# Optimization experiments

Measured on AMD Instinct MI355X. Metric: run time of the kernel, lower is better.

Reference implementation:

```python
import jax, jax.numpy as jnp
import numpy as np

N = 20000
E = 320000
NEG_SLOPE = 0.2
LN_EPS = 1e-5


def gat_conv(x, W, a_src, a_dst, b, src, dst, heads, ch, concat):
    # x: [N, F_in]; W: [F_in, H*C]; a_src/a_dst: [H, C]; b: [H*C] or [C]
    xl = (x @ W).reshape(N, heads, ch)                      # [N,H,C]
    alpha_src = jnp.sum(xl * a_src, axis=-1)                # [N,H]
    alpha_dst = jnp.sum(xl * a_dst, axis=-1)                # [N,H]
    e = alpha_src[src] + alpha_dst[dst]                     # [E',H]
    e = jax.nn.leaky_relu(e, NEG_SLOPE)
    # segment softmax over incoming edges of each dst node
    m = jax.ops.segment_max(e, dst, num_segments=N)         # [N,H]
    m = jnp.where(jnp.isfinite(m), m, 0.0)
    ex = jnp.exp(e - m[dst])
    denom = jax.ops.segment_sum(ex, dst, num_segments=N)    # [N,H]
    alpha = ex / (denom[dst] + 1e-16)                       # [E',H]
    msg = alpha[:, :, None] * xl[src]                       # [E',H,C]
    out = jax.ops.segment_sum(msg, dst, num_segments=N)     # [N,H,C]
    if concat:
        return out.reshape(N, heads * ch) + b
    return out.mean(axis=1) + b


def layer_norm(x, g, b):
    mu = jnp.mean(x, axis=-1, keepdims=True)
    var = jnp.mean(jnp.square(x - mu), axis=-1, keepdims=True)
    return (x - mu) * jax.lax.rsqrt(var + LN_EPS) * g + b


def setup_inputs() -> dict:
    key = jax.random.key(0)
    ks = jax.random.split(key, 24)
    d = {}
    d["x"] = jax.random.normal(ks[0], (N, 50), dtype=jnp.float32)
    d["edge_index"] = jax.random.randint(ks[1], (2, E), 0, N, dtype=jnp.int64)

    def glorot(k, shape):
        fan = shape[0] + shape[-1]
        return jax.random.normal(k, shape, dtype=jnp.float32) * np.sqrt(2.0 / fan)

    # conv1: 50 -> 256, heads=4, concat
    d["W1"] = glorot(ks[2], (50, 4 * 256))
    d["a_src1"] = glorot(ks[3], (4, 256))
    d["a_dst1"] = glorot(ks[4], (4, 256))
    d["b1"] = jnp.zeros((4 * 256,), jnp.float32)
    # conv2: 1024 -> 256, heads=4, concat
    d["W2"] = glorot(ks[5], (1024, 4 * 256))
    d["a_src2"] = glorot(ks[6], (4, 256))
    d["a_dst2"] = glorot(ks[7], (4, 256))
    d["b2"] = jnp.zeros((4 * 256,), jnp.float32)
    # conv3: 1024 -> 121, heads=6, concat=False
    d["W3"] = glorot(ks[8], (1024, 6 * 121))
    d["a_src3"] = glorot(ks[9], (6, 121))
    d["a_dst3"] = glorot(ks[10], (6, 121))
    d["b3"] = jnp.zeros((121,), jnp.float32)
    # skips
    d["skipW1"] = glorot(ks[11], (50, 1024))
    d["skipb1"] = jnp.zeros((1024,), jnp.float32)
    d["skipW2"] = glorot(ks[12], (1024, 1024))
    d["skipb2"] = jnp.zeros((1024,), jnp.float32)
    # layer norms
    d["g1"] = jnp.ones((1024,), jnp.float32)
    d["beta1"] = jnp.zeros((1024,), jnp.float32)
    d["g2"] = jnp.ones((1024,), jnp.float32)
    d["beta2"] = jnp.zeros((1024,), jnp.float32)
    return d


def reference(x, edge_index, W1, a_src1, a_dst1, b1, W2, a_src2, a_dst2, b2,
              W3, a_src3, a_dst3, b3, skipW1, skipb1, skipW2, skipb2,
              g1, beta1, g2, beta2):
    # add self loops (PyG GATConv default)
    loop = jnp.arange(N, dtype=edge_index.dtype)
    src = jnp.concatenate([edge_index[0], loop])
    dst = jnp.concatenate([edge_index[1], loop])

    h = gat_conv(x, W1, a_src1, a_dst1, b1, src, dst, 4, 256, True)
    h = jax.nn.elu(layer_norm(h + (x @ skipW1 + skipb1), g1, beta1))
    h2 = gat_conv(h, W2, a_src2, a_dst2, b2, src, dst, 4, 256, True)
    h2 = jax.nn.elu(layer_norm(h2 + (h @ skipW2 + skipb2), g2, beta2))
    out = gat_conv(h2, W3, a_src3, a_dst3, b3, src, dst, 6, 121, False)
    return out
```

## Files before the change

### kernel.cpp

```cpp
#include <hip/hip_runtime.h>
#include <hip/hip_bf16.h>
#include <math.h>

typedef __attribute__((ext_vector_type(8))) __bf16 bf16x8;
typedef __attribute__((ext_vector_type(2))) __bf16 bf16x2;
typedef __attribute__((ext_vector_type(4))) float f32x4;

#define LSTR 40

__global__ __launch_bounds__(256) void gemm_bt(const __bf16* __restrict__ A,
                                               const __bf16* __restrict__ Bt,
                                               __bf16* __restrict__ C,
                                               int M, int N, int K) {
    __shared__ __bf16 As[128 * LSTR];
    __shared__ __bf16 Bs[128 * LSTR];
    const int t = threadIdx.x;
    const int lane = t & 63;
    const int wid = t >> 6;
    const int wm = (wid >> 1) << 6;
    const int wn = (wid & 1) << 6;
    const int bm = blockIdx.x * 128;
    const int bn = blockIdx.y * 128;

    const int lr = t >> 2;
    const int lc = (t & 3) << 3;

    f32x4 acc[4][4];
#pragma unroll
    for (int i = 0; i < 4; i++)
#pragma unroll
        for (int j = 0; j < 4; j++) acc[i][j] = (f32x4){0.f, 0.f, 0.f, 0.f};

    const int m16 = lane & 15;
    const int k8 = (lane >> 4) << 3;

    for (int k0 = 0; k0 < K; k0 += 32) {
        bf16x8 a0 = *(const bf16x8*)(A + (size_t)(bm + lr) * K + k0 + lc);
        bf16x8 a1 = *(const bf16x8*)(A + (size_t)(bm + lr + 64) * K + k0 + lc);
        bf16x8 b0 = *(const bf16x8*)(Bt + (size_t)(bn + lr) * K + k0 + lc);
        bf16x8 b1 = *(const bf16x8*)(Bt + (size_t)(bn + lr + 64) * K + k0 + lc);
        __syncthreads();
        *(bf16x8*)(As + lr * LSTR + lc) = a0;
        *(bf16x8*)(As + (lr + 64) * LSTR + lc) = a1;
        *(bf16x8*)(Bs + lr * LSTR + lc) = b0;
        *(bf16x8*)(Bs + (lr + 64) * LSTR + lc) = b1;
        __syncthreads();
        bf16x8 af[4], bfr[4];
#pragma unroll
        for (int i = 0; i < 4; i++) {
            af[i] = *(const bf16x8*)(As + (wm + 16 * i + m16) * LSTR + k8);
            bfr[i] = *(const bf16x8*)(Bs + (wn + 16 * i + m16) * LSTR + k8);
        }
#pragma unroll
        for (int i = 0; i < 4; i++)
#pragma unroll
            for (int j = 0; j < 4; j++)
                acc[i][j] = __builtin_amdgcn_mfma_f32_16x16x32_bf16(af[i], bfr[j], acc[i][j], 0, 0, 0);
    }
    const int r4 = (lane >> 4) << 2;
#pragma unroll
    for (int i = 0; i < 4; i++) {
#pragma unroll
        for (int j = 0; j < 4; j++) {
            int col = bn + wn + 16 * j + m16;
#pragma unroll
            for (int r = 0; r < 4; r++) {
                int row = bm + wm + 16 * i + r4 + r;
                C[(size_t)row * N + col] = (__bf16)acc[i][j][r];
            }
        }
    }
}

__global__ void pack_x_k(const float* __restrict__ x, __bf16* __restrict__ xp, int rows_real) {
    int i = blockIdx.x * 256 + threadIdx.x;
    int n = i >> 6, c = i & 63;
    float v = 0.f;
    if (n < rows_real && c < 50) v = x[n * 50 + c];
    xp[(size_t)n * 64 + c] = (__bf16)v;
}

__global__ void transpose_pad_k(const float* __restrict__ W, __bf16* __restrict__ WT,
                                int K, int N, int Kp, int Np) {
    __shared__ float tile[32][33];
    int bx = blockIdx.x, by = blockIdx.y;
    int tx = threadIdx.x & 31, ty = threadIdx.x >> 5;
#pragma unroll
    for (int r = ty; r < 32; r += 8) {
        int k = by * 32 + r, n = bx * 32 + tx;
        float v = 0.f;
        if (k < K && n < N) v = W[(size_t)k * N + n];
        tile[r][tx] = v;
    }
    __syncthreads();
#pragma unroll
    for (int r = ty; r < 32; r += 8) {
        int n = bx * 32 + r, k = by * 32 + tx;
        if (n < Np && k < Kp) WT[(size_t)n * Kp + k] = (__bf16)tile[tx][r];
    }
}

__global__ void probe_ei_k(const int* __restrict__ ei, int* __restrict__ flag) {
    if (blockIdx.x == 0 && threadIdx.x == 0) {
        int all0 = 1;
        for (int i = 0; i < 64; i++)
            if (ei[2 * i + 1] != 0) { all0 = 0; break; }
        *flag = all0;
    }
}

__device__ __forceinline__ int load_ei(const int* ei, int idx, int is64) {
    return is64 ? ei[2 * idx] : ei[idx];
}

__global__ void hist_k(const int* __restrict__ ei, const int* __restrict__ flag,
                       int* __restrict__ cnt, int E, int Nn) {
    int e = blockIdx.x * 256 + threadIdx.x;
    if (e >= E + Nn) return;
    int is64 = *flag;
    int d = (e < E) ? load_ei(ei, E + e, is64) : (e - E);
    d = min(max(d, 0), Nn - 1);
    atomicAdd(&cnt[d], 1);
}

__global__ __launch_bounds__(1024) void scan_k(const int* __restrict__ cnt, int* __restrict__ row_ptr,
                                               int Nn, int total) {
    __shared__ int part[1024];
    int t = threadIdx.x;
    int chunk = (Nn + 1023) >> 10;
    int lo = t * chunk;
    int hi = lo + chunk; if (hi > Nn) hi = Nn; if (lo > Nn) lo = Nn;
    int s = 0;
    for (int i = lo; i < hi; i++) s += cnt[i];
    part[t] = s;
    __syncthreads();
    for (int off = 1; off < 1024; off <<= 1) {
        int v = (t >= off) ? part[t - off] : 0;
        __syncthreads();
        part[t] += v;
        __syncthreads();
    }
    int run = part[t] - s;
    for (int i = lo; i < hi; i++) { row_ptr[i] = run; run += cnt[i]; }
    if (t == 0) row_ptr[Nn] = total;
}

__global__ void fill_csr_k(const int* __restrict__ ei, const int* __restrict__ flag,
                           const int* __restrict__ row_ptr, int* __restrict__ cursor,
                           int* __restrict__ src_csr, int E, int Nn) {
    int e = blockIdx.x * 256 + threadIdx.x;
    if (e >= E + Nn) return;
    int is64 = *flag;
    int d = (e < E) ? load_ei(ei, E + e, is64) : (e - E);
    int s = (e < E) ? load_ei(ei, e, is64) : (e - E);
    d = min(max(d, 0), Nn - 1);
    s = min(max(s, 0), Nn - 1);
    int slot = row_ptr[d] + atomicAdd(&cursor[d], 1);
    src_csr[slot] = s;
}

__global__ void alpha_k(const __bf16* __restrict__ XL, int ld, const float* __restrict__ a_src,
                        const float* __restrict__ a_dst, float* __restrict__ asrc,
                        float* __restrict__ adst, int Nn, int H, int C, int Cpad) {
    int gw = (blockIdx.x * 256 + threadIdx.x) >> 6;
    int lane = threadIdx.x & 63;
    if (gw >= Nn * H) return;
    int n = gw / H, h = gw - n * H;
    const __bf16* row = XL + (size_t)n * ld + h * Cpad;
    const float* as = a_src + h * C;
    const float* ad = a_dst + h * C;
    float s = 0.f, d = 0.f;
    for (int c = lane; c < C; c += 64) {
        float v = (float)row[c];
        s += v * as[c];
        d += v * ad[c];
    }
#pragma unroll
    for (int off = 32; off; off >>= 1) {
        s += __shfl_down(s, off);
        d += __shfl_down(d, off);
    }
    if (lane == 0) { asrc[n * H + h] = s; adst[n * H + h] = d; }
}

__global__ void attn_k(const int* __restrict__ row_ptr, const int* __restrict__ src_csr,
                       const float* __restrict__ asrc, const float* __restrict__ adst,
                       float* __restrict__ w, int Nn, int H) {
    int gw = (blockIdx.x * 256 + threadIdx.x) >> 6;
    int lane = threadIdx.x & 63;
    if (gw >= Nn) return;
    int n = gw;
    int base = row_ptr[n], deg = row_ptr[n + 1] - base;
    for (int h = 0; h < H; h++) {
        float ad = adst[n * H + h];
        float m = -1e30f;
        for (int s = lane; s < deg; s += 64) {
            float e = asrc[src_csr[base + s] * H + h] + ad;
            e = e > 0.f ? e : 0.2f * e;
            m = fmaxf(m, e);
        }
#pragma unroll
        for (int off = 1; off < 64; off <<= 1) m = fmaxf(m, __shfl_xor(m, off));
        float sum = 0.f;
        for (int s = lane; s < deg; s += 64) {
            float e = asrc[src_csr[base + s] * H + h] + ad;
            e = e > 0.f ? e : 0.2f * e;
            sum += __expf(e - m);
        }
#pragma unroll
        for (int off = 1; off < 64; off <<= 1) sum += __shfl_xor(sum, off);
        float inv = 1.f / (sum + 1e-16f);
        for (int s = lane; s < deg; s += 64) {
            float e = asrc[src_csr[base + s] * H + h] + ad;
            e = e > 0.f ? e : 0.2f * e;
            w[(size_t)(base + s) * H + h] = __expf(e - m) * inv;
        }
    }
}

__global__ __launch_bounds__(256) void agg_skip4(const __bf16* __restrict__ XL,
                                                 const float* __restrict__ w,
                                                 const int* __restrict__ row_ptr,
                                                 const int* __restrict__ src_csr,
                                                 const float* __restrict__ bias,
                                                 const float* __restrict__ sb,
                                                 __bf16* __restrict__ SK, int Nn) {
    const int cc = blockIdx.x;
    const int n = blockIdx.y * 4 + (threadIdx.x >> 6);
    const int lane = threadIdx.x & 63;
    if (n >= Nn) return;
    const int g = lane >> 4;
    const int p = lane & 15;
    const int col = cc * 128 + p * 8;
    const int head = cc >> 1;
    const int base = row_ptr[n], end = row_ptr[n + 1];

    float acc[8];
#pragma unroll
    for (int j = 0; j < 8; j++) acc[j] = 0.f;

    for (int e = base; e < end; e += 8) {
        int ea = e + g, eb = e + g + 4;
        bool va = ea < end, vb = eb < end;
        int sa = va ? src_csr[ea] : src_csr[base];
        int sb2 = vb ? src_csr[eb] : src_csr[base];
        float wa = va ? w[(size_t)ea * 4 + head] : 0.f;
        float wb = vb ? w[(size_t)eb * 4 + head] : 0.f;
        bf16x8 xa = *(const bf16x8*)(XL + (size_t)sa * 1024 + col);
        bf16x8 xb = *(const bf16x8*)(XL + (size_t)sb2 * 1024 + col);
#pragma unroll
        for (int j = 0; j < 8; j++) acc[j] += wa * (float)xa[j] + wb * (float)xb[j];
    }
#pragma unroll
    for (int j = 0; j < 8; j++) {
        acc[j] += __shfl_xor(acc[j], 16);
        acc[j] += __shfl_xor(acc[j], 32);
    }
    if (lane < 16) {
        size_t o = (size_t)n * 1024 + col;
        bf16x8 sk = *(const bf16x8*)(SK + o);
        bf16x8 res;
#pragma unroll
        for (int j = 0; j < 8; j++)
            res[j] = (__bf16)(acc[j] + bias[col + j] + sb[col + j] + (float)sk[j]);
        *(bf16x8*)(SK + o) = res;
    }
}

__global__ __launch_bounds__(256) void agg_mean4(const __bf16* __restrict__ XL,
                                                 const float* __restrict__ w,
                                                 const int* __restrict__ row_ptr,
                                                 const int* __restrict__ src_csr,
                                                 __bf16* __restrict__ part, int Nn) {
    const int cc = blockIdx.x;
    const int n = blockIdx.y * 4 + (threadIdx.x >> 6);
    const int lane = threadIdx.x & 63;
    if (n >= Nn) return;
    const int g = lane >> 4;
    const int p = lane & 15;
    int col = cc * 96 + p * 8;
    if (col > 760) col = 760;
    const int h0 = col / 121;
    int h1 = (col + 7) / 121;
    if (h1 > 5) h1 = 5;
    bool hi[8];
#pragma unroll
    for (int j = 0; j < 8; j++) hi[j] = ((col + j) / 121) > h0;
    const int base = row_ptr[n], end = row_ptr[n + 1];

    float acc[8];
#pragma unroll
    for (int j = 0; j < 8; j++) acc[j] = 0.f;

    for (int e = base; e < end; e += 8) {
        int ea = e + g, eb = e + g + 4;
        bool va = ea < end, vb = eb < end;
        int sa = va ? src_csr[ea] : src_csr[base];
        int sb2 = vb ? src_csr[eb] : src_csr[base];
        const float* wpa = w + (size_t)ea * 6;
        const float* wpb = w + (size_t)eb * 6;
        float wa0 = va ? wpa[h0] : 0.f, wa1 = va ? wpa[h1] : 0.f;
        float wb0 = vb ? wpb[h0] : 0.f, wb1 = vb ? wpb[h1] : 0.f;
        bf16x8 xa = *(const bf16x8*)(XL + (size_t)sa * 768 + col);
        bf16x8 xb = *(const bf16x8*)(XL + (size_t)sb2 * 768 + col);
#pragma unroll
        for (int j = 0; j < 8; j++) {
            float wja = hi[j] ? wa1 : wa0;
            float wjb = hi[j] ? wb1 : wb0;
            acc[j] += wja * (float)xa[j] + wjb * (float)xb[j];
        }
    }
#pragma unroll
    for (int j = 0; j < 8; j++) {
        acc[j] += __shfl_xor(acc[j], 16);
        acc[j] += __shfl_xor(acc[j], 32);
    }
    if (lane < 12) {
        size_t o = (size_t)n * 768 + cc * 96 + lane * 8;
        bf16x8 res;
#pragma unroll
        for (int j = 0; j < 8; j++) res[j] = (__bf16)acc[j];
        *(bf16x8*)(part + o) = res;
    }
}

__global__ __launch_bounds__(128) void reduce_mean_k(const __bf16* __restrict__ part,
                                                     const float* __restrict__ b3,
                                                     float* __restrict__ out, int Nn) {
    int n = blockIdx.x;
    int t = threadIdx.x;
    if (t >= 121) return;
    const __bf16* row = part + (size_t)n * 768;
    float s = 0.f;
#pragma unroll
    for (int h = 0; h < 6; h++) s += (float)row[h * 121 + t];
    out[(size_t)n * 121 + t] = s * (1.f / 6.f) + b3[t];
}

__global__ __launch_bounds__(256) void ln_elu_k(const __bf16* __restrict__ in,
                                                const float* __restrict__ g,
                                                const float* __restrict__ be,
                                                __bf16* __restrict__ out, int rows_real) {
    const int D = 1024;
    int n = blockIdx.x;
    int t = threadIdx.x;
    size_t ro = (size_t)n * D;
    if (n >= rows_real) {
#pragma unroll
        for (int j = 0; j < 4; j++) out[ro + t + 256 * j] = (__bf16)0.f;
        return;
    }
    float v[4];
    float s = 0.f, q = 0.f;
#pragma unroll
    for (int j = 0; j < 4; j++) {
        int c = t + 256 * j;
        float a = (float)in[ro + c];
        v[j] = a;
        s += a;
        q += a * a;
    }
#pragma unroll
    for (int off = 32; off; off >>= 1) {
        s += __shfl_down(s, off);
        q += __shfl_down(q, off);
    }
    __shared__ float rs[8];
    int wid = t >> 6;
    if ((t & 63) == 0) { rs[wid] = s; rs[wid + 4] = q; }
    __syncthreads();
    s = rs[0] + rs[1] + rs[2] + rs[3];
    q = rs[4] + rs[5] + rs[6] + rs[7];
    float mu = s * (1.f / 1024.f);
    float var = q * (1.f / 1024.f) - mu * mu;
    float inv = rsqrtf(fmaxf(var, 0.f) + 1e-5f);
#pragma unroll
    for (int j = 0; j < 4; j++) {
        int c = t + 256 * j;
        float y = (v[j] - mu) * inv * g[c] + be[c];
        y = y > 0.f ? y : expm1f(y);
        out[ro + c] = (__bf16)y;
    }
}

extern "C" void kernel_launch(void* const* d_in, const int* in_sizes, int n_in,
                              void* d_out, int out_size, void* d_ws, size_t ws_size,
                              hipStream_t stream) {
    const float* x   = (const float*)d_in[0];
    const int*   ei  = (const int*)d_in[1];
    const float* W1  = (const float*)d_in[2];
    const float* as1 = (const float*)d_in[3];
    const float* ad1 = (const float*)d_in[4];
    const float* b1  = (const float*)d_in[5];
    const float* W2  = (const float*)d_in[6];
    const float* as2 = (const float*)d_in[7];
    const float* ad2 = (const float*)d_in[8];
    const float* b2  = (const float*)d_in[9];
    const float* W3  = (const float*)d_in[10];
    const float* as3 = (const float*)d_in[11];
    const float* ad3 = (const float*)d_in[12];
    const float* b3  = (const float*)d_in[13];
    const float* sW1 = (const float*)d_in[14];
    const float* sb1 = (const float*)d_in[15];
    const float* sW2 = (const float*)d_in[16];
    const float* sb2 = (const float*)d_in[17];
    const float* g1  = (const float*)d_in[18];
    const float* be1 = (const float*)d_in[19];
    const float* g2  = (const float*)d_in[20];
    const float* be2 = (const float*)d_in[21];
    float* out = (float*)d_out;

    const int Nn = 20000;
    const int E = in_sizes[1] / 2;
    const int E2 = E + Nn;
    const int Mpad = 20096;

    char* p = (char*)d_ws;
    auto alloc = [&](size_t bytes) {
        char* r = p;
        p += (bytes + 255) & ~(size_t)255;
        return r;
    };
    __bf16* W1pT  = (__bf16*)alloc((size_t)1024 * 64 * 2);
    __bf16* sW1T  = (__bf16*)alloc((size_t)1024 * 64 * 2);
    __bf16* W2T   = (__bf16*)alloc((size_t)1024 * 1024 * 2);
    __bf16* sW2T  = (__bf16*)alloc((size_t)1024 * 1024 * 2);
    __bf16* W3pT  = (__bf16*)alloc((size_t)768 * 1024 * 2);
    __bf16* xp    = (__bf16*)alloc((size_t)Mpad * 64 * 2);
    __bf16* XL    = (__bf16*)alloc((size_t)Mpad * 1024 * 2);
    __bf16* SK    = (__bf16*)alloc((size_t)Mpad * 1024 * 2);
    __bf16* H1    = (__bf16*)alloc((size_t)Mpad * 1024 * 2);
    float*  asrcb = (float*)alloc((size_t)Nn * 6 * 4);
    float*  adstb = (float*)alloc((size_t)Nn * 6 * 4);
    float*  wbuf  = (float*)alloc((size_t)E2 * 6 * 4);
    int*    rowp  = (int*)alloc((size_t)(Nn + 1) * 4);
    int*    cnt   = (int*)alloc((size_t)Nn * 4);
    int*    scsr  = (int*)alloc((size_t)E2 * 4);
    int*    eiflag= (int*)alloc(256);
    __bf16* part  = SK;
    (void)ws_size; (void)n_in; (void)out_size;

    pack_x_k<<<(Mpad * 64) / 256, 256, 0, stream>>>(x, xp, Nn);
    transpose_pad_k<<<dim3(32, 2), 256, 0, stream>>>(W1, W1pT, 50, 1024, 64, 1024);
    transpose_pad_k<<<dim3(32, 2), 256, 0, stream>>>(sW1, sW1T, 50, 1024, 64, 1024);
    transpose_pad_k<<<dim3(32, 32), 256, 0, stream>>>(W2, W2T, 1024, 1024, 1024, 1024);
    transpose_pad_k<<<dim3(32, 32), 256, 0, stream>>>(sW2, sW2T, 1024, 1024, 1024, 1024);
    transpose_pad_k<<<dim3(24, 32), 256, 0, stream>>>(W3, W3pT, 1024, 726, 1024, 768);

    probe_ei_k<<<1, 64, 0, stream>>>(ei, eiflag);
    hipMemsetAsync(cnt, 0, (size_t)Nn * 4, stream);
    hist_k<<<(E2 + 255) / 256, 256, 0, stream>>>(ei, eiflag, cnt, E, Nn);
    scan_k<<<1, 1024, 0, stream>>>(cnt, rowp, Nn, E2);
    hipMemsetAsync(cnt, 0, (size_t)Nn * 4, stream);
    fill_csr_k<<<(E2 + 255) / 256, 256, 0, stream>>>(ei, eiflag, rowp, cnt, scsr, E, Nn);

    gemm_bt<<<dim3(Mpad / 128, 8), 256, 0, stream>>>(xp, W1pT, XL, Mpad, 1024, 64);
    gemm_bt<<<dim3(Mpad / 128, 8), 256, 0, stream>>>(xp, sW1T, SK, Mpad, 1024, 64);
    alpha_k<<<(Nn * 4 * 64) / 256, 256, 0, stream>>>(XL, 1024, as1, ad1, asrcb, adstb, Nn, 4, 256, 256);
    attn_k<<<(Nn + 3) / 4, 256, 0, stream>>>(rowp, scsr, asrcb, adstb, wbuf, Nn, 4);
    agg_skip4<<<dim3(8, (Nn + 3) / 4), 256, 0, stream>>>(XL, wbuf, rowp, scsr, b1, sb1, SK, Nn);
    ln_elu_k<<<Mpad, 256, 0, stream>>>(SK, g1, be1, H1, Nn);

    gemm_bt<<<dim3(Mpad / 128, 8), 256, 0, stream>>>(H1, W2T, XL, Mpad, 1024, 1024);
    gemm_bt<<<dim3(Mpad / 128, 8), 256, 0, stream>>>(H1, sW2T, SK, Mpad, 1024, 1024);
    alpha_k<<<(Nn * 4 * 64) / 256, 256, 0, stream>>>(XL, 1024, as2, ad2, asrcb, adstb, Nn, 4, 256, 256);
    attn_k<<<(Nn + 3) / 4, 256, 0, stream>>>(rowp, scsr, asrcb, adstb, wbuf, Nn, 4);
    agg_skip4<<<dim3(8, (Nn + 3) / 4), 256, 0, stream>>>(XL, wbuf, rowp, scsr, b2, sb2, SK, Nn);
    ln_elu_k<<<Mpad, 256, 0, stream>>>(SK, g2, be2, H1, Nn);

    gemm_bt<<<dim3(Mpad / 128, 6), 256, 0, stream>>>(H1, W3pT, XL, Mpad, 768, 1024);
    alpha_k<<<(Nn * 6 * 64) / 256, 256, 0, stream>>>(XL, 768, as3, ad3, asrcb, adstb, Nn, 6, 121, 121);
    attn_k<<<(Nn + 3) / 4, 256, 0, stream>>>(rowp, scsr, asrcb, adstb, wbuf, Nn, 6);
    agg_mean4<<<dim3(8, (Nn + 3) / 4), 256, 0, stream>>>(XL, wbuf, rowp, scsr, part, Nn);
    reduce_mean_k<<<Nn, 128, 0, stream>>>(part, b3, out, Nn);
}
```

Baseline: 869.6 us.

## Use direct global-to-LDS loads in GEMM, pad layer-3 heads, widen aggregation

```diff
diff --git a/kernel.cpp b/kernel.cpp
--- a/kernel.cpp
+++ b/kernel.cpp
@@ -3,17 +3,24 @@
 #include <math.h>
 
 typedef __attribute__((ext_vector_type(8))) __bf16 bf16x8;
-typedef __attribute__((ext_vector_type(2))) __bf16 bf16x2;
 typedef __attribute__((ext_vector_type(4))) float f32x4;
 
-#define LSTR 40
+#if __has_builtin(__builtin_amdgcn_global_load_lds)
+#define HAVE_GLD 1
+#define GLD16(g, l)                                                                      \
+    __builtin_amdgcn_global_load_lds(                                                    \
+        (const __attribute__((address_space(1))) unsigned int*)(g),                      \
+        (__attribute__((address_space(3))) unsigned int*)(l), 16, 0, 0)
+#else
+#define HAVE_GLD 0
+#endif
 
 __global__ __launch_bounds__(256) void gemm_bt(const __bf16* __restrict__ A,
                                                const __bf16* __restrict__ Bt,
                                                __bf16* __restrict__ C,
                                                int M, int N, int K) {
-    __shared__ __bf16 As[128 * LSTR];
-    __shared__ __bf16 Bs[128 * LSTR];
+    __shared__ __bf16 As[128 * 32];
+    __shared__ __bf16 Bs[128 * 32];
     const int t = threadIdx.x;
     const int lane = t & 63;
     const int wid = t >> 6;
@@ -22,8 +29,8 @@
     const int bm = blockIdx.x * 128;
     const int bn = blockIdx.y * 128;
 
-    const int lr = t >> 2;
-    const int lc = (t & 3) << 3;
+    const int srow = (wid << 4) + (lane >> 2);
+    const int scol = (lane & 3) << 3;
 
     f32x4 acc[4][4];
 #pragma unroll
@@ -35,21 +42,30 @@
     const int k8 = (lane >> 4) << 3;
 
     for (int k0 = 0; k0 < K; k0 += 32) {
-        bf16x8 a0 = *(const bf16x8*)(A + (size_t)(bm + lr) * K + k0 + lc);
-        bf16x8 a1 = *(const bf16x8*)(A + (size_t)(bm + lr + 64) * K + k0 + lc);
-        bf16x8 b0 = *(const bf16x8*)(Bt + (size_t)(bn + lr) * K + k0 + lc);
-        bf16x8 b1 = *(const bf16x8*)(Bt + (size_t)(bn + lr + 64) * K + k0 + lc);
         __syncthreads();
-        *(bf16x8*)(As + lr * LSTR + lc) = a0;
-        *(bf16x8*)(As + (lr + 64) * LSTR + lc) = a1;
-        *(bf16x8*)(Bs + lr * LSTR + lc) = b0;
-        *(bf16x8*)(Bs + (lr + 64) * LSTR + lc) = b1;
+#if HAVE_GLD
+        GLD16(A + (size_t)(bm + srow) * K + k0 + scol, As + srow * 32 + scol);
+        GLD16(A + (size_t)(bm + 64 + srow) * K + k0 + scol, As + (64 + srow) * 32 + scol);
+        GLD16(Bt + (size_t)(bn + srow) * K + k0 + scol, Bs + srow * 32 + scol);
+        GLD16(Bt + (size_t)(bn + 64 + srow) * K + k0 + scol, Bs + (64 + srow) * 32 + scol);
+#else
+        {
+            bf16x8 a0 = *(const bf16x8*)(A + (size_t)(bm + srow) * K + k0 + scol);
+            bf16x8 a1 = *(const bf16x8*)(A + (size_t)(bm + 64 + srow) * K + k0 + scol);
+            bf16x8 b0 = *(const bf16x8*)(Bt + (size_t)(bn + srow) * K + k0 + scol);
+            bf16x8 b1 = *(const bf16x8*)(Bt + (size_t)(bn + 64 + srow) * K + k0 + scol);
+            *(bf16x8*)(As + srow * 32 + scol) = a0;
+            *(bf16x8*)(As + (64 + srow) * 32 + scol) = a1;
+            *(bf16x8*)(Bs + srow * 32 + scol) = b0;
+            *(bf16x8*)(Bs + (64 + srow) * 32 + scol) = b1;
+        }
+#endif
         __syncthreads();
         bf16x8 af[4], bfr[4];
 #pragma unroll
         for (int i = 0; i < 4; i++) {
-            af[i] = *(const bf16x8*)(As + (wm + 16 * i + m16) * LSTR + k8);
-            bfr[i] = *(const bf16x8*)(Bs + (wn + 16 * i + m16) * LSTR + k8);
+            af[i] = *(const bf16x8*)(As + (wm + 16 * i + m16) * 32 + k8);
+            bfr[i] = *(const bf16x8*)(Bs + (wn + 16 * i + m16) * 32 + k8);
         }
 #pragma unroll
         for (int i = 0; i < 4; i++)
@@ -97,6 +113,30 @@
     for (int r = ty; r < 32; r += 8) {
         int n = bx * 32 + r, k = by * 32 + tx;
         if (n < Np && k < Kp) WT[(size_t)n * Kp + k] = (__bf16)tile[tx][r];
+    }
+}
+
+__global__ void transpose_pad_w3_k(const float* __restrict__ W, __bf16* __restrict__ WT) {
+    __shared__ float tile[32][33];
+    int bx = blockIdx.x, by = blockIdx.y;
+    int tx = threadIdx.x & 31, ty = threadIdx.x >> 5;
+    int r0 = bx * 32;
+    int h = r0 >> 7;
+    int c0 = r0 & 127;
+#pragma unroll
+    for (int r = ty; r < 32; r += 8) {
+        int k = by * 32 + r;
+        int c = c0 + tx;
+        float v = 0.f;
+        if (c < 121) v = W[(size_t)k * 726 + h * 121 + c];
+        tile[r][tx] = v;
+    }
+    __syncthreads();
+#pragma unroll
+    for (int r = ty; r < 32; r += 8) {
+        int rr = r0 + r;
+        int k = by * 32 + tx;
+        WT[(size_t)rr * 1024 + k] = (__bf16)tile[tx][r];
     }
 }
 
@@ -218,7 +258,7 @@
     }
 }
 
-__global__ __launch_bounds__(256) void agg_skip4(const __bf16* __restrict__ XL,
+__global__ __launch_bounds__(256) void agg_skip5(const __bf16* __restrict__ XL,
                                                  const float* __restrict__ w,
                                                  const int* __restrict__ row_ptr,
                                                  const int* __restrict__ src_csr,
@@ -239,17 +279,22 @@
 #pragma unroll
     for (int j = 0; j < 8; j++) acc[j] = 0.f;
 
-    for (int e = base; e < end; e += 8) {
-        int ea = e + g, eb = e + g + 4;
-        bool va = ea < end, vb = eb < end;
-        int sa = va ? src_csr[ea] : src_csr[base];
-        int sb2 = vb ? src_csr[eb] : src_csr[base];
-        float wa = va ? w[(size_t)ea * 4 + head] : 0.f;
-        float wb = vb ? w[(size_t)eb * 4 + head] : 0.f;
-        bf16x8 xa = *(const bf16x8*)(XL + (size_t)sa * 1024 + col);
-        bf16x8 xb = *(const bf16x8*)(XL + (size_t)sb2 * 1024 + col);
-#pragma unroll
-        for (int j = 0; j < 8; j++) acc[j] += wa * (float)xa[j] + wb * (float)xb[j];
+    for (int e = base; e < end; e += 16) {
+        int sidx[4];
+        float wv[4];
+#pragma unroll
+        for (int s = 0; s < 4; s++) {
+            int idx = e + g + 4 * s;
+            bool v = idx < end;
+            sidx[s] = v ? src_csr[idx] : src_csr[base];
+            wv[s] = v ? w[(size_t)idx * 4 + head] : 0.f;
+        }
+#pragma unroll
+        for (int s = 0; s < 4; s++) {
+            bf16x8 xv = *(const bf16x8*)(XL + (size_t)sidx[s] * 1024 + col);
+#pragma unroll
+            for (int j = 0; j < 8; j++) acc[j] += wv[s] * (float)xv[j];
+        }
     }
 #pragma unroll
     for (int j = 0; j < 8; j++) {
@@ -267,7 +312,7 @@
     }
 }
 
-__global__ __launch_bounds__(256) void agg_mean4(const __bf16* __restrict__ XL,
+__global__ __launch_bounds__(256) void agg_mean5(const __bf16* __restrict__ XL,
                                                  const float* __restrict__ w,
                                                  const int* __restrict__ row_ptr,
                                                  const int* __restrict__ src_csr,
@@ -278,36 +323,28 @@
     if (n >= Nn) return;
     const int g = lane >> 4;
     const int p = lane & 15;
-    int col = cc * 96 + p * 8;
-    if (col > 760) col = 760;
-    const int h0 = col / 121;
-    int h1 = (col + 7) / 121;
-    if (h1 > 5) h1 = 5;
-    bool hi[8];
-#pragma unroll
-    for (int j = 0; j < 8; j++) hi[j] = ((col + j) / 121) > h0;
+    const int col = cc * 128 + p * 8;
     const int base = row_ptr[n], end = row_ptr[n + 1];
 
     float acc[8];
 #pragma unroll
     for (int j = 0; j < 8; j++) acc[j] = 0.f;
 
-    for (int e = base; e < end; e += 8) {
-        int ea = e + g, eb = e + g + 4;
-        bool va = ea < end, vb = eb < end;
-        int sa = va ? src_csr[ea] : src_csr[base];
-        int sb2 = vb ? src_csr[eb] : src_csr[base];
-        const float* wpa = w + (size_t)ea * 6;
-        const float* wpb = w + (size_t)eb * 6;
-        float wa0 = va ? wpa[h0] : 0.f, wa1 = va ? wpa[h1] : 0.f;
-        float wb0 = vb ? wpb[h0] : 0.f, wb1 = vb ? wpb[h1] : 0.f;
-        bf16x8 xa = *(const bf16x8*)(XL + (size_t)sa * 768 + col);
-        bf16x8 xb = *(const bf16x8*)(XL + (size_t)sb2 * 768 + col);
-#pragma unroll
-        for (int j = 0; j < 8; j++) {
-            float wja = hi[j] ? wa1 : wa0;
-            float wjb = hi[j] ? wb1 : wb0;
-            acc[j] += wja * (float)xa[j] + wjb * (float)xb[j];
+    for (int e = base; e < end; e += 16) {
+        int sidx[4];
+        float wv[4];
+#pragma unroll
+        for (int s = 0; s < 4; s++) {
+            int idx = e + g + 4 * s;
+            bool v = idx < end;
+            sidx[s] = v ? src_csr[idx] : src_csr[base];
+            wv[s] = v ? w[(size_t)idx * 6 + cc] : 0.f;
+        }
+#pragma unroll
+        for (int s = 0; s < 4; s++) {
+            bf16x8 xv = *(const bf16x8*)(XL + (size_t)sidx[s] * 768 + col);
+#pragma unroll
+            for (int j = 0; j < 8; j++) acc[j] += wv[s] * (float)xv[j];
         }
     }
 #pragma unroll
@@ -315,8 +352,8 @@
         acc[j] += __shfl_xor(acc[j], 16);
         acc[j] += __shfl_xor(acc[j], 32);
     }
-    if (lane < 12) {
-        size_t o = (size_t)n * 768 + cc * 96 + lane * 8;
+    if (lane < 16) {
+        size_t o = (size_t)n * 768 + col;
         bf16x8 res;
 #pragma unroll
         for (int j = 0; j < 8; j++) res[j] = (__bf16)acc[j];
@@ -333,7 +370,7 @@
     const __bf16* row = part + (size_t)n * 768;
     float s = 0.f;
 #pragma unroll
-    for (int h = 0; h < 6; h++) s += (float)row[h * 121 + t];
+    for (int h = 0; h < 6; h++) s += (float)row[h * 128 + t];
     out[(size_t)n * 121 + t] = s * (1.f / 6.f) + b3[t];
 }
 
@@ -445,7 +482,7 @@
     transpose_pad_k<<<dim3(32, 2), 256, 0, stream>>>(sW1, sW1T, 50, 1024, 64, 1024);
     transpose_pad_k<<<dim3(32, 32), 256, 0, stream>>>(W2, W2T, 1024, 1024, 1024, 1024);
     transpose_pad_k<<<dim3(32, 32), 256, 0, stream>>>(sW2, sW2T, 1024, 1024, 1024, 1024);
-    transpose_pad_k<<<dim3(24, 32), 256, 0, stream>>>(W3, W3pT, 1024, 726, 1024, 768);
+    transpose_pad_w3_k<<<dim3(24, 32), 256, 0, stream>>>(W3, W3pT);
 
     probe_ei_k<<<1, 64, 0, stream>>>(ei, eiflag);
     hipMemsetAsync(cnt, 0, (size_t)Nn * 4, stream);
@@ -458,19 +495,19 @@
     gemm_bt<<<dim3(Mpad / 128, 8), 256, 0, stream>>>(xp, sW1T, SK, Mpad, 1024, 64);
     alpha_k<<<(Nn * 4 * 64) / 256, 256, 0, stream>>>(XL, 1024, as1, ad1, asrcb, adstb, Nn, 4, 256, 256);
     attn_k<<<(Nn + 3) / 4, 256, 0, stream>>>(rowp, scsr, asrcb, adstb, wbuf, Nn, 4);
-    agg_skip4<<<dim3(8, (Nn + 3) / 4), 256, 0, stream>>>(XL, wbuf, rowp, scsr, b1, sb1, SK, Nn);
+    agg_skip5<<<dim3(8, (Nn + 3) / 4), 256, 0, stream>>>(XL, wbuf, rowp, scsr, b1, sb1, SK, Nn);
     ln_elu_k<<<Mpad, 256, 0, stream>>>(SK, g1, be1, H1, Nn);
 
     gemm_bt<<<dim3(Mpad / 128, 8), 256, 0, stream>>>(H1, W2T, XL, Mpad, 1024, 1024);
     gemm_bt<<<dim3(Mpad / 128, 8), 256, 0, stream>>>(H1, sW2T, SK, Mpad, 1024, 1024);
     alpha_k<<<(Nn * 4 * 64) / 256, 256, 0, stream>>>(XL, 1024, as2, ad2, asrcb, adstb, Nn, 4, 256, 256);
     attn_k<<<(Nn + 3) / 4, 256, 0, stream>>>(rowp, scsr, asrcb, adstb, wbuf, Nn, 4);
-    agg_skip4<<<dim3(8, (Nn + 3) / 4), 256, 0, stream>>>(XL, wbuf, rowp, scsr, b2, sb2, SK, Nn);
+    agg_skip5<<<dim3(8, (Nn + 3) / 4), 256, 0, stream>>>(XL, wbuf, rowp, scsr, b2, sb2, SK, Nn);
     ln_elu_k<<<Mpad, 256, 0, stream>>>(SK, g2, be2, H1, Nn);
 
     gemm_bt<<<dim3(Mpad / 128, 6), 256, 0, stream>>>(H1, W3pT, XL, Mpad, 768, 1024);
-    alpha_k<<<(Nn * 6 * 64) / 256, 256, 0, stream>>>(XL, 768, as3, ad3, asrcb, adstb, Nn, 6, 121, 121);
+    alpha_k<<<(Nn * 6 * 64) / 256, 256, 0, stream>>>(XL, 768, as3, ad3, asrcb, adstb, Nn, 6, 121, 128);
     attn_k<<<(Nn + 3) / 4, 256, 0, stream>>>(rowp, scsr, asrcb, adstb, wbuf, Nn, 6);
-    agg_mean4<<<dim3(8, (Nn + 3) / 4), 256, 0, stream>>>(XL, wbuf, rowp, scsr, part, Nn);
+    agg_mean5<<<dim3(6, (Nn + 3) / 4), 256, 0, stream>>>(XL, wbuf, rowp, scsr, part, Nn);
     reduce_mean_k<<<Nn, 128, 0, stream>>>(part, b3, out, Nn);
 }
```

After: 851.2 us. -2.1%, faster.
